# Optimization experiments

Measured on AMD Instinct MI355X. Metric: run time of the kernel, lower is better.

## Reference

```python
import jax, jax.numpy as jnp
import numpy as np

C = 1024
GROUPS = 32
EPS = 1e-5
K = 20


def group_norm(v, weight, bias):
    # v: [B, C]; normalize per group of C//GROUPS channels (torch GroupNorm on 2D input)
    B = v.shape[0]
    g = v.reshape(B, GROUPS, C // GROUPS)
    mean = g.mean(axis=-1, keepdims=True)
    var = g.var(axis=-1, keepdims=True)
    g = (g - mean) * jax.lax.rsqrt(var + EPS)
    return g.reshape(B, C) * weight + bias


def setup_inputs() -> dict:
    key = jax.random.key(0)
    ks = jax.random.split(key, 16)
    B, L = 32, 2048
    s = 1.0 / np.sqrt(C)
    inp = {
        "x": jax.random.normal(ks[0], (B, L, C), dtype=jnp.float32),
        "W": jax.random.uniform(ks[1], (C, C), jnp.float32, -s, s),
        "b": jax.random.uniform(ks[2], (C,), jnp.float32, -s, s),
        "W1": jax.random.uniform(ks[3], (C, C), jnp.float32, -s, s),
        "b1": jax.random.uniform(ks[4], (C,), jnp.float32, -s, s),
        "Wm": jax.random.uniform(ks[5], (C, C), jnp.float32, -s, s),
        "bm": jax.random.uniform(ks[6], (C,), jnp.float32, -s, s),
        "Wa": jax.random.uniform(ks[7], (C, C), jnp.float32, -s, s),
        "ba": jax.random.uniform(ks[8], (C,), jnp.float32, -s, s),
        "g1_w": jnp.ones((C,), jnp.float32),
        "g1_b": jnp.zeros((C,), jnp.float32),
        "g2_w": jnp.ones((C,), jnp.float32),
        "g2_b": jnp.zeros((C,), jnp.float32),
    }
    return inp


def reference(x, W, b, W1, b1, Wm, bm, Wa, ba, g1_w, g1_b, g2_w, g2_b):
    # x: [B, L, C]
    x = jnp.einsum('blc,dc->bld', x, W) + b          # self.linear
    x_M = x.mean(axis=1)                              # adaptive avg pool over L -> [B, C]
    x_M = group_norm(x_M @ Wm.T + bm, g1_w, g1_b)     # linear_max + gn1
    x_A = x.max(axis=1)                               # adaptive max pool over L -> [B, C]
    x_A = group_norm(x_A @ Wa.T + ba, g2_w, g2_b)     # linear_Aug + gn2
    x = jnp.einsum('blc,dc->bld', x, W1) + b1         # self.linear1
    out1 = jnp.einsum('blc,bc->bl', x, x_M)           # x @ x_M^T, squeezed
    out2 = jnp.einsum('blc,bc->bl', x, x_A)
    out = jax.nn.softmax(out1, axis=1) * jax.nn.softmax(out2, axis=1)  # [B, L]
    _, topk_idx = jax.lax.top_k(out, K)               # [B, K]
    selected = jnp.take_along_axis(x, topk_idx[:, :, None], axis=1)  # [B, K, C]
    return selected
```

## Files before the change

### kernel.cpp

```cpp
#include <hip/hip_runtime.h>

#define L_SEQ 2048
#define CH    1024
#define NB    32
#define KSEL  20

typedef short v8s  __attribute__((ext_vector_type(8)));
typedef float v16f __attribute__((ext_vector_type(16)));

#define WS_XSUM   0
#define WS_YMAX   32768
#define WS_M1     65536
#define WS_AMAX   98304
#define WS_T1     131072
#define WS_T2     163840
#define WS_P      196608
#define WS_V      294912
#define WS_S      327680
#define WS_TOPK   393216
#define WS_BC     394240
#define WS_WC     395264
#define WS_WPAK   1443840
#define WS_WTPAK  2492416

__device__ __forceinline__ void split8(float4 qa, float4 qb, uint4& hi, uint4& lo) {
  float f[8] = {qa.x, qa.y, qa.z, qa.w, qb.x, qb.y, qb.z, qb.w};
  unsigned h[8], l[8];
  #pragma unroll
  for (int e = 0; e < 8; ++e) {
    unsigned u  = __float_as_uint(f[e]);
    unsigned hu = u & 0xFFFF0000u;
    float lf    = f[e] - __uint_as_float(hu);
    h[e] = u >> 16;
    l[e] = __float_as_uint(lf) >> 16;
  }
  hi.x = h[0] | (h[1] << 16); hi.y = h[2] | (h[3] << 16);
  hi.z = h[4] | (h[5] << 16); hi.w = h[6] | (h[7] << 16);
  lo.x = l[0] | (l[1] << 16); lo.y = l[2] | (l[3] << 16);
  lo.z = l[4] | (l[5] << 16); lo.w = l[6] | (l[7] << 16);
}

__device__ __forceinline__ void pack_row_body(const float* __restrict__ W,
                                              uint4* __restrict__ wp,
                                              int Rw, int kt, int t) {
  const float* wb = W + (size_t)Rw * 128 * CH;
  uint4* out = wp + ((size_t)Rw * 32 + kt) * 1024;
  #pragma unroll
  for (int pass = 0; pass < 2; ++pass) {
    int idx = pass * 256 + t;
    int r = idx >> 2, p = idx & 3;
    const float* ap = wb + (size_t)r * CH + kt * 32 + p * 8;
    float4 f0 = *(const float4*)ap;
    float4 f1 = *(const float4*)(ap + 4);
    uint4 hi, lo;
    split8(f0, f1, hi, lo);
    int slot = ((r >> 5) * 2 + (p >> 1)) * 128 + (p & 1) * 32 + (r & 31);
    out[slot] = hi;
    out[slot + 64] = lo;
  }
}

__device__ __forceinline__ void pack_tr_body(const float* __restrict__ W,
                                             uint4* __restrict__ wtp,
                                             int cc, int kt, int t,
                                             float (*__restrict__ Wl)[129]) {
  #pragma unroll
  for (int it = 0; it < 16; ++it) {
    int idx = it * 256 + t;
    int el = idx >> 7, cl = idx & 127;
    Wl[el][cl] = W[(size_t)(kt * 32 + el) * CH + cc * 128 + cl];
  }
  __syncthreads();
  uint4* out = wtp + ((size_t)cc * 32 + kt) * 1024;
  #pragma unroll
  for (int pass = 0; pass < 2; ++pass) {
    int sid = pass * 256 + t;
    int r = sid >> 2, p = sid & 3;
    float f[8];
    #pragma unroll
    for (int q = 0; q < 8; ++q) f[q] = Wl[p * 8 + q][r];
    float4 f0 = {f[0], f[1], f[2], f[3]}, f1 = {f[4], f[5], f[6], f[7]};
    uint4 hi, lo;
    split8(f0, f1, hi, lo);
    int slot = ((r >> 5) * 2 + (p >> 1)) * 128 + (p & 1) * 32 + (r & 31);
    out[slot] = hi;
    out[slot + 64] = lo;
  }
}

__global__ __launch_bounds__(256) void prep_kernel(const float* __restrict__ W,
                                                   const float* __restrict__ W1,
                                                   const float* __restrict__ b,
                                                   const float* __restrict__ b1,
                                                   uint4* __restrict__ wp,
                                                   uint4* __restrict__ wtp,
                                                   float* __restrict__ wsf,
                                                   float* __restrict__ bc) {
  __shared__ float Wl[32][129];
  int t = threadIdx.x, x = blockIdx.x, y = blockIdx.y;
  if (y < 8) {
    int flat = (y * 32 + x) * 256 + t;
    wsf[WS_XSUM + flat] = 0.f;
    if (flat < 32768) wsf[WS_V + flat] = 0.f;
    pack_row_body(W, wp, y, x, t);
  } else if (y < 16) {
    int tid = ((y - 8) * 32 + x) * 256 + t;
    float4* wc4 = (float4*)(wsf + WS_WC);
    #pragma unroll
    for (int r = 0; r < 4; ++r) wc4[(size_t)tid * 4 + r] = float4{0.f, 0.f, 0.f, 0.f};
    pack_tr_body(W, wtp, y - 8, x, t, Wl);
  } else {
    int bk = (y - 16) * 32 + x;
    int d = bk * 8 + (t >> 5);
    int lane = t & 31;
    const float4* wr = (const float4*)(W1 + (size_t)d * CH);
    const float4* br = (const float4*)b;
    float acc = 0.f;
    #pragma unroll
    for (int c = lane; c < 256; c += 32) {
      float4 a = wr[c], m = br[c];
      acc += a.x * m.x + a.y * m.y + a.z * m.z + a.w * m.w;
    }
    #pragma unroll
    for (int off = 16; off; off >>= 1) acc += __shfl_xor(acc, off);
    if (lane == 0) bc[d] = acc + b1[d];
  }
}

__global__ __launch_bounds__(256) void packw_kernel(const float* __restrict__ W,
                                                    uint4* __restrict__ wp) {
  pack_row_body(W, wp, blockIdx.y, blockIdx.x, threadIdx.x);
}

__global__ __launch_bounds__(256) void mean_kernel(const float* __restrict__ x,
                                                   float* __restrict__ xsum) {
  int b = blockIdx.y, chunk = blockIdx.x, t = threadIdx.x;
  const float4* bp = (const float4*)(x + ((size_t)b * L_SEQ + (size_t)chunk * 64) * CH);
  float sx = 0.f, sy = 0.f, sz = 0.f, sw = 0.f;
  #pragma unroll 4
  for (int l = 0; l < 64; ++l) {
    float4 a = bp[l * 256 + t];
    sx += a.x; sy += a.y; sz += a.z; sw += a.w;
  }
  float* dst = xsum + b * CH + t * 4;
  atomicAdd(dst + 0, sx); atomicAdd(dst + 1, sy);
  atomicAdd(dst + 2, sz); atomicAdd(dst + 3, sw);
}

template<bool FOURTH, int NKT>
__device__ __forceinline__ void gemm_core(const float* __restrict__ arow,
                                          const uint4* __restrict__ wbB,
                                          const int cgbase,
                                          uint4 (*__restrict__ smA)[1024],
                                          const int w, const int lane,
                                          v16f acc[4][2]) {
  {
    float4 p0 = *(const float4*)(arow);
    float4 p1 = *(const float4*)(arow + 4);
    float4 p2 = *(const float4*)(arow + 16);
    float4 p3 = *(const float4*)(arow + 20);
    uint4 hi, lo;
    split8(p0, p1, hi, lo);
    smA[0][(w * 2 + 0) * 128 + lane] = hi;
    smA[0][(w * 2 + 0) * 128 + 64 + lane] = lo;
    split8(p2, p3, hi, lo);
    smA[0][(w * 2 + 1) * 128 + lane] = hi;
    smA[0][(w * 2 + 1) * 128 + 64 + lane] = lo;
  }
  v8s bc[4], bn[4];
  #pragma unroll
  for (int j = 0; j < 2; ++j) {
    bc[j * 2]     = *(const v8s*)&wbB[((cgbase + j) * 2 + 0) * 128];
    bc[j * 2 + 1] = *(const v8s*)&wbB[((cgbase + j) * 2 + 0) * 128 + 64];
  }
  __syncthreads();

  for (int kt = 0; kt < NKT; ++kt) {
    const int cur = kt & 1;
    float4 q0, q1, q2, q3;
    if (kt < NKT - 1) {
      const float* an = arow + (kt + 1) * 32;
      q0 = *(const float4*)(an);
      q1 = *(const float4*)(an + 4);
      q2 = *(const float4*)(an + 16);
      q3 = *(const float4*)(an + 20);
    }
    #pragma unroll
    for (int s = 0; s < 2; ++s) {
      const int nkt = s ? kt + 1 : kt, ns = s ^ 1;
      if (nkt < NKT) {
        #pragma unroll
        for (int j = 0; j < 2; ++j) {
          bn[j * 2]     = *(const v8s*)&wbB[(size_t)nkt * 1024 + ((cgbase + j) * 2 + ns) * 128];
          bn[j * 2 + 1] = *(const v8s*)&wbB[(size_t)nkt * 1024 + ((cgbase + j) * 2 + ns) * 128 + 64];
        }
      }
      v8s ah[4], al[4];
      #pragma unroll
      for (int i = 0; i < 4; ++i) {
        int base = (i * 2 + s) * 128 + lane;
        ah[i] = *(const v8s*)&smA[cur][base];
        al[i] = *(const v8s*)&smA[cur][base + 64];
      }
      #pragma unroll
      for (int j = 0; j < 2; ++j) {
        v8s bh = bc[j * 2], bl = bc[j * 2 + 1];
        #pragma unroll
        for (int i = 0; i < 4; ++i) {
          acc[i][j] = __builtin_amdgcn_mfma_f32_32x32x16_bf16(ah[i], bh, acc[i][j], 0, 0, 0);
          acc[i][j] = __builtin_amdgcn_mfma_f32_32x32x16_bf16(ah[i], bl, acc[i][j], 0, 0, 0);
          acc[i][j] = __builtin_amdgcn_mfma_f32_32x32x16_bf16(al[i], bh, acc[i][j], 0, 0, 0);
          if (FOURTH)
            acc[i][j] = __builtin_amdgcn_mfma_f32_32x32x16_bf16(al[i], bl, acc[i][j], 0, 0, 0);
        }
      }
      #pragma unroll
      for (int e = 0; e < 4; ++e) bc[e] = bn[e];
    }
    if (kt < NKT - 1) {
      uint4 hi, lo;
      split8(q0, q1, hi, lo);
      smA[cur ^ 1][(w * 2 + 0) * 128 + lane] = hi;
      smA[cur ^ 1][(w * 2 + 0) * 128 + 64 + lane] = lo;
      split8(q2, q3, hi, lo);
      smA[cur ^ 1][(w * 2 + 1) * 128 + lane] = hi;
      smA[cur ^ 1][(w * 2 + 1) * 128 + 64 + lane] = lo;
    }
    __syncthreads();
  }
}

__global__ __launch_bounds__(256, 2) void gemm_max5(const float* __restrict__ X,
                                                    const uint4* __restrict__ wp,
                                                    unsigned* __restrict__ ymax) {
  __shared__ uint4 smA[2][1024];
  const int t = threadIdx.x, lane = t & 63, w = t >> 6;
  const int blk = blockIdx.x;
  const int strip = blk & 3, mt = blk >> 2;
  const int batch = mt >> 4;
  const float* arow = X + (size_t)(mt * 128 + w * 32 + (lane & 31)) * CH + (lane >> 5) * 8;
  v16f acc[4][2];
  #pragma unroll
  for (int i = 0; i < 4; ++i)
    #pragma unroll
    for (int j = 0; j < 2; ++j)
      #pragma unroll
      for (int e = 0; e < 16; ++e) acc[i][j][e] = 0.f;
  const uint4* wbB = wp + (size_t)(strip * 2 + (w >> 1)) * 32768 + lane;
  gemm_core<false, 32>(arow, wbB, (w & 1) * 2, smA, w, lane, acc);

  #pragma unroll
  for (int j = 0; j < 2; ++j) {
    float m = -INFINITY;
    #pragma unroll
    for (int i = 0; i < 4; ++i)
      #pragma unroll
      for (int e = 0; e < 16; ++e) m = fmaxf(m, acc[i][j][e]);
    m = fmaxf(m, __shfl_xor(m, 32));
    if (lane < 32) {
      int col = strip * 256 + w * 64 + j * 32 + lane;
      unsigned u = __float_as_uint(m);
      unsigned enc = (m >= 0.f) ? (u | 0x80000000u) : ~u;
      atomicMax(&ymax[batch * CH + col], enc);
    }
  }
}

__global__ __launch_bounds__(256, 2) void wc_gemm(const float* __restrict__ W1,
                                                  const uint4* __restrict__ wtp,
                                                  float* __restrict__ Wc) {
  __shared__ uint4 smA[2][1024];
  const int t = threadIdx.x, lane = t & 63, w = t >> 6;
  const int blk = blockIdx.x, chunk = blockIdx.y;
  const int strip = blk & 3, mt = blk >> 2;
  const float* arow = W1 + (size_t)(mt * 128 + w * 32 + (lane & 31)) * CH
                         + (lane >> 5) * 8 + chunk * 256;
  v16f acc[4][2];
  #pragma unroll
  for (int i = 0; i < 4; ++i)
    #pragma unroll
    for (int j = 0; j < 2; ++j)
      #pragma unroll
      for (int e = 0; e < 16; ++e) acc[i][j][e] = 0.f;
  const uint4* wbB = wtp + (size_t)(strip * 2 + (w >> 1)) * 32768
                         + (size_t)chunk * (8 * 1024) + lane;
  gemm_core<true, 8>(arow, wbB, (w & 1) * 2, smA, w, lane, acc);

  #pragma unroll
  for (int i = 0; i < 4; ++i)
    #pragma unroll
    for (int j = 0; j < 2; ++j)
      #pragma unroll
      for (int r = 0; r < 16; ++r) {
        int row = (r & 3) + 8 * (r >> 2) + 4 * (lane >> 5);
        int grow = mt * 128 + i * 32 + row;
        int gcol = strip * 256 + w * 64 + j * 32 + (lane & 31);
        atomicAdd(&Wc[(size_t)grow * CH + gcol], acc[i][j][r]);
      }
}

__global__ __launch_bounds__(256, 2) void out_gemm(const float* __restrict__ X,
                                                   const int* __restrict__ idx,
                                                   const uint4* __restrict__ wcp,
                                                   float* __restrict__ C) {
  __shared__ uint4 smA[2][1024];
  const int t = threadIdx.x, lane = t & 63, w = t >> 6;
  const int blk = blockIdx.x, chunk = blockIdx.y;
  const int strip = blk & 3, mt = blk >> 2;
  const int rr = mt * 128 + w * 32 + (lane & 31);
  const int grow_a = (rr / KSEL) * L_SEQ + idx[rr];
  const float* arow = X + (size_t)grow_a * CH + (lane >> 5) * 8 + chunk * 128;
  v16f acc[4][2];
  #pragma unroll
  for (int i = 0; i < 4; ++i)
    #pragma unroll
    for (int j = 0; j < 2; ++j)
      #pragma unroll
      for (int e = 0; e < 16; ++e) acc[i][j][e] = 0.f;
  const uint4* wbB = wcp + (size_t)(strip * 2 + (w >> 1)) * 32768
                         + (size_t)chunk * (4 * 1024) + lane;
  gemm_core<true, 4>(arow, wbB, (w & 1) * 2, smA, w, lane, acc);

  #pragma unroll
  for (int i = 0; i < 4; ++i)
    #pragma unroll
    for (int j = 0; j < 2; ++j)
      #pragma unroll
      for (int r = 0; r < 16; ++r) {
        int row = (r & 3) + 8 * (r >> 2) + 4 * (lane >> 5);
        int grow = mt * 128 + i * 32 + row;
        int gcol = strip * 256 + w * 64 + j * 32 + (lane & 31);
        atomicAdd(&C[(size_t)grow * CH + gcol], acc[i][j][r]);
      }
}

__global__ __launch_bounds__(256) void poolmix_kernel(const float* __restrict__ xsum,
                                                      const unsigned* __restrict__ ymax,
                                                      const float* __restrict__ W,
                                                      const float* __restrict__ bias,
                                                      float* __restrict__ m1,
                                                      float* __restrict__ amax) {
  int t = threadIdx.x;
  int id = blockIdx.x * 256 + t;
  unsigned u = ymax[id];
  float f = (u & 0x80000000u) ? __uint_as_float(u & 0x7FFFFFFFu) : __uint_as_float(~u);
  amax[id] = f + bias[id & (CH - 1)];

  int d = blockIdx.x * 8 + (t >> 5);
  int b = t & 31;
  const float4* Ir = (const float4*)(xsum + b * CH);
  const float4* Mr = (const float4*)(W + (size_t)d * CH);
  float acc = 0.f;
  #pragma unroll 4
  for (int c = 0; c < CH / 4; ++c) {
    float4 a = Ir[c], m = Mr[c];
    acc += a.x * m.x + a.y * m.y + a.z * m.z + a.w * m.w;
  }
  m1[b * CH + d] = acc * (1.f / 2048.f) + bias[d];
}

__global__ __launch_bounds__(256) void lin2_kernel(const float* __restrict__ m1,
                                                   const float* __restrict__ amax,
                                                   const float* __restrict__ Wm,
                                                   const float* __restrict__ bm,
                                                   const float* __restrict__ Wa,
                                                   const float* __restrict__ ba,
                                                   float* __restrict__ t1,
                                                   float* __restrict__ t2) {
  int t = threadIdx.x;
  int which = blockIdx.x >> 7, bk = blockIdx.x & 127;
  const float* I = which ? amax : m1;
  const float* M = which ? Wa : Wm;
  const float* bb = which ? ba : bm;
  float* O = which ? t2 : t1;
  int d = bk * 8 + (t >> 5);
  int b = t & 31;
  const float4* Ir = (const float4*)(I + b * CH);
  const float4* Mr = (const float4*)(M + (size_t)d * CH);
  float acc = 0.f;
  #pragma unroll 4
  for (int c = 0; c < CH / 4; ++c) {
    float4 a = Ir[c], m = Mr[c];
    acc += a.x * m.x + a.y * m.y + a.z * m.z + a.w * m.w;
  }
  O[b * CH + d] = acc + bb[d];
}

__global__ __launch_bounds__(1024) void gnp_kernel(const float* __restrict__ t1,
                                                   const float* __restrict__ t2,
                                                   const float* __restrict__ g1w, const float* __restrict__ g1b,
                                                   const float* __restrict__ g2w, const float* __restrict__ g2b,
                                                   float* __restrict__ p,
                                                   const float* __restrict__ bc,
                                                   float* __restrict__ dout) {
  int b = blockIdx.x, c = threadIdx.x;
  float v1 = t1[b * CH + c], v2 = t2[b * CH + c];
  float s1 = v1, s2 = v2;
  #pragma unroll
  for (int off = 16; off; off >>= 1) { s1 += __shfl_xor(s1, off); s2 += __shfl_xor(s2, off); }
  float d1 = v1 - s1 * (1.f / 32.f), d2 = v2 - s2 * (1.f / 32.f);
  float q1 = d1 * d1, q2 = d2 * d2;
  #pragma unroll
  for (int off = 16; off; off >>= 1) { q1 += __shfl_xor(q1, off); q2 += __shfl_xor(q2, off); }
  float o1 = d1 * rsqrtf(q1 * (1.f / 32.f) + 1e-5f) * g1w[c] + g1b[c];
  float o2 = d2 * rsqrtf(q2 * (1.f / 32.f) + 1e-5f) * g2w[c] + g2b[c];
  p[b * CH + c] = o1 + o2;

  int g = b * CH + c;
  float bcc = bc[c];
  #pragma unroll
  for (int r = 0; r < KSEL; ++r) dout[(size_t)r * (NB * CH) + g] = bcc;
}

__global__ __launch_bounds__(256) void colmm_kernel(const float* __restrict__ S,
                                                    const float* __restrict__ M,
                                                    float* __restrict__ O) {
  __shared__ float Sl[128][32];
  int t = threadIdx.x;
  int e0 = (blockIdx.x & 3) * 256, c0 = (blockIdx.x >> 2) * 128;
  for (int i = t; i < 4096; i += 256) {
    int c = i >> 5, b = i & 31;
    Sl[c][b] = S[b * CH + c0 + c];
  }
  __syncthreads();
  int e = e0 + t;
  float acc[32];
  #pragma unroll
  for (int b = 0; b < 32; ++b) acc[b] = 0.f;
  for (int c = 0; c < 128; ++c) {
    float wv = M[(size_t)(c0 + c) * CH + e];
    #pragma unroll
    for (int b = 0; b < 32; ++b) acc[b] += Sl[c][b] * wv;
  }
  #pragma unroll
  for (int b = 0; b < 32; ++b) atomicAdd(&O[b * CH + e], acc[b]);
}

__global__ __launch_bounds__(256) void logits_kernel(const float* __restrict__ x,
                                                     const float* __restrict__ v,
                                                     float* __restrict__ s) {
  __shared__ float4 vl[256];
  int b = blockIdx.y, chunk = blockIdx.x, t = threadIdx.x;
  vl[t] = ((const float4*)(v + b * CH))[t];
  __syncthreads();
  int wv = t >> 6, lane = t & 63;
  for (int it = 0; it < 8; ++it) {
    int l = chunk * 32 + it * 4 + wv;
    const float4* xr = (const float4*)(x + ((size_t)b * L_SEQ + l) * CH);
    float acc = 0.f;
    #pragma unroll
    for (int rep = 0; rep < 4; ++rep) {
      float4 a = xr[rep * 64 + lane];
      float4 c = vl[rep * 64 + lane];
      acc += a.x * c.x + a.y * c.y + a.z * c.z + a.w * c.w;
    }
    #pragma unroll
    for (int off = 32; off; off >>= 1) acc += __shfl_xor(acc, off);
    if (lane == 0) s[b * L_SEQ + l] = acc;
  }
}

__global__ __launch_bounds__(256) void topk_kernel(const float* __restrict__ s,
                                                   int* __restrict__ idx_out) {
  int b = blockIdx.x, t = threadIdx.x;
  int lane = t & 63, w = t >> 6;
  __shared__ float lv[4];
  __shared__ int   li[4];
  float v[8];
  #pragma unroll
  for (int j = 0; j < 8; ++j) v[j] = s[b * L_SEQ + j * 256 + t];
  for (int k = 0; k < KSEL; ++k) {
    float bv = -INFINITY; int bi = 1 << 30;
    #pragma unroll
    for (int j = 0; j < 8; ++j) {
      int gi = j * 256 + t;
      if (v[j] > bv || (v[j] == bv && gi < bi)) { bv = v[j]; bi = gi; }
    }
    #pragma unroll
    for (int off = 32; off; off >>= 1) {
      float ov = __shfl_xor(bv, off); int oi = __shfl_xor(bi, off);
      if (ov > bv || (ov == bv && oi < bi)) { bv = ov; bi = oi; }
    }
    if (lane == 0) { lv[w] = bv; li[w] = bi; }
    __syncthreads();
    float fv = lv[0]; int fi = li[0];
    #pragma unroll
    for (int w2 = 1; w2 < 4; ++w2) {
      float ov = lv[w2]; int oi = li[w2];
      if (ov > fv || (ov == fv && oi < fi)) { fv = ov; fi = oi; }
    }
    if (t == 0) idx_out[b * KSEL + k] = fi;
    if ((fi & 255) == t) v[fi >> 8] = -INFINITY;
    __syncthreads();
  }
}

extern "C" void kernel_launch(void* const* d_in, const int* in_sizes, int n_in,
                              void* d_out, int out_size, void* d_ws, size_t ws_size,
                              hipStream_t stream) {
  const float* x   = (const float*)d_in[0];
  const float* W   = (const float*)d_in[1];
  const float* b   = (const float*)d_in[2];
  const float* W1  = (const float*)d_in[3];
  const float* b1  = (const float*)d_in[4];
  const float* Wm  = (const float*)d_in[5];
  const float* bm  = (const float*)d_in[6];
  const float* Wa  = (const float*)d_in[7];
  const float* ba  = (const float*)d_in[8];
  const float* g1w = (const float*)d_in[9];
  const float* g1b = (const float*)d_in[10];
  const float* g2w = (const float*)d_in[11];
  const float* g2b = (const float*)d_in[12];

  float* wsf = (float*)d_ws;
  float*    xsum = wsf + WS_XSUM;
  unsigned* ymax = (unsigned*)(wsf + WS_YMAX);
  float*    m1   = wsf + WS_M1;
  float*    amax = wsf + WS_AMAX;
  float*    t1   = wsf + WS_T1;
  float*    t2   = wsf + WS_T2;
  float*    p    = wsf + WS_P;
  float*    vvec = wsf + WS_V;
  float*    sbuf = wsf + WS_S;
  int*      tidx = (int*)(wsf + WS_TOPK);
  float*    bcv  = wsf + WS_BC;
  float*    Wc   = wsf + WS_WC;
  uint4*    wpak = (uint4*)(wsf + WS_WPAK);
  uint4*    wtpak = (uint4*)(wsf + WS_WTPAK);

  prep_kernel<<<dim3(32, 20), 256, 0, stream>>>(W, W1, b, b1, wpak, wtpak, wsf, bcv);
  mean_kernel<<<dim3(32, 32), 256, 0, stream>>>(x, xsum);
  gemm_max5<<<2048, 256, 0, stream>>>(x, wpak, ymax);

  wc_gemm<<<dim3(32, 4), 256, 0, stream>>>(W1, wtpak, Wc);
  packw_kernel<<<dim3(32, 8), 256, 0, stream>>>(Wc, wtpak);

  poolmix_kernel<<<128, 256, 0, stream>>>(xsum, ymax, W, b, m1, amax);
  lin2_kernel<<<256, 256, 0, stream>>>(m1, amax, Wm, bm, Wa, ba, t1, t2);
  gnp_kernel<<<32, 1024, 0, stream>>>(t1, t2, g1w, g1b, g2w, g2b, p, bcv, (float*)d_out);
  colmm_kernel<<<32, 256, 0, stream>>>(p, Wc, vvec);
  logits_kernel<<<dim3(64, 32), 256, 0, stream>>>(x, vvec, sbuf);
  topk_kernel<<<32, 256, 0, stream>>>(sbuf, tidx);
  out_gemm<<<dim3(20, 8), 256, 0, stream>>>(x, tidx, wtpak, (float*)d_out);
}
```

Before: 963.0 us.

## Merge mean, max-GEMM and Wc GEMM into one interleaved launch; fuse pack with poolmix

Three independent kernels (the column-sum of x, the projected max GEMM, and the W1*W product GEMM) become one 3200-block launch. Each group of 25 blocks holds 16 GEMM tiles, 8 mean chunks and 1 Wc tile, so the bandwidth-bound and MFMA-bound work share the GPU at the same time. The Wc packing and the pooled-linear kernel are merged into a second launch. Inside the GEMM core, the next A-tile is now written to shared memory after the first k-substep instead of after the whole inner loop. This gives earlier LDS writes and somewhat more overlap, at the cost of heterogeneous blocks that may unbalance occupancy and register use.

```diff
diff --git a/kernel.cpp b/kernel.cpp
--- a/kernel.cpp
+++ b/kernel.cpp
@@ -125,26 +125,6 @@
     for (int off = 16; off; off >>= 1) acc += __shfl_xor(acc, off);
     if (lane == 0) bc[d] = acc + b1[d];
   }
-}
-
-__global__ __launch_bounds__(256) void packw_kernel(const float* __restrict__ W,
-                                                    uint4* __restrict__ wp) {
-  pack_row_body(W, wp, blockIdx.y, blockIdx.x, threadIdx.x);
-}
-
-__global__ __launch_bounds__(256) void mean_kernel(const float* __restrict__ x,
-                                                   float* __restrict__ xsum) {
-  int b = blockIdx.y, chunk = blockIdx.x, t = threadIdx.x;
-  const float4* bp = (const float4*)(x + ((size_t)b * L_SEQ + (size_t)chunk * 64) * CH);
-  float sx = 0.f, sy = 0.f, sz = 0.f, sw = 0.f;
-  #pragma unroll 4
-  for (int l = 0; l < 64; ++l) {
-    float4 a = bp[l * 256 + t];
-    sx += a.x; sy += a.y; sz += a.z; sw += a.w;
-  }
-  float* dst = xsum + b * CH + t * 4;
-  atomicAdd(dst + 0, sx); atomicAdd(dst + 1, sy);
-  atomicAdd(dst + 2, sz); atomicAdd(dst + 3, sw);
 }
 
 template<bool FOURTH, int NKT>
@@ -216,87 +196,104 @@
       }
       #pragma unroll
       for (int e = 0; e < 4; ++e) bc[e] = bn[e];
-    }
-    if (kt < NKT - 1) {
-      uint4 hi, lo;
-      split8(q0, q1, hi, lo);
-      smA[cur ^ 1][(w * 2 + 0) * 128 + lane] = hi;
-      smA[cur ^ 1][(w * 2 + 0) * 128 + 64 + lane] = lo;
-      split8(q2, q3, hi, lo);
-      smA[cur ^ 1][(w * 2 + 1) * 128 + lane] = hi;
-      smA[cur ^ 1][(w * 2 + 1) * 128 + 64 + lane] = lo;
+      if (s == 0 && kt < NKT - 1) {
+        uint4 hi, lo;
+        split8(q0, q1, hi, lo);
+        smA[cur ^ 1][(w * 2 + 0) * 128 + lane] = hi;
+        smA[cur ^ 1][(w * 2 + 0) * 128 + 64 + lane] = lo;
+        split8(q2, q3, hi, lo);
+        smA[cur ^ 1][(w * 2 + 1) * 128 + lane] = hi;
+        smA[cur ^ 1][(w * 2 + 1) * 128 + 64 + lane] = lo;
+      }
     }
     __syncthreads();
   }
 }
 
-__global__ __launch_bounds__(256, 2) void gemm_max5(const float* __restrict__ X,
-                                                    const uint4* __restrict__ wp,
-                                                    unsigned* __restrict__ ymax) {
+__global__ __launch_bounds__(256, 2) void fused3_kernel(const float* __restrict__ X,
+                                                        const uint4* __restrict__ wp,
+                                                        unsigned* __restrict__ ymax,
+                                                        float* __restrict__ xsum,
+                                                        const float* __restrict__ W1,
+                                                        const uint4* __restrict__ wtp,
+                                                        float* __restrict__ Wc) {
   __shared__ uint4 smA[2][1024];
+  const int id = blockIdx.x;
+  const int g = id / 25, r = id % 25;
   const int t = threadIdx.x, lane = t & 63, w = t >> 6;
-  const int blk = blockIdx.x;
-  const int strip = blk & 3, mt = blk >> 2;
-  const int batch = mt >> 4;
-  const float* arow = X + (size_t)(mt * 128 + w * 32 + (lane & 31)) * CH + (lane >> 5) * 8;
-  v16f acc[4][2];
-  #pragma unroll
-  for (int i = 0; i < 4; ++i)
-    #pragma unroll
-    for (int j = 0; j < 2; ++j)
-      #pragma unroll
-      for (int e = 0; e < 16; ++e) acc[i][j][e] = 0.f;
-  const uint4* wbB = wp + (size_t)(strip * 2 + (w >> 1)) * 32768 + lane;
-  gemm_core<false, 32>(arow, wbB, (w & 1) * 2, smA, w, lane, acc);
-
-  #pragma unroll
-  for (int j = 0; j < 2; ++j) {
-    float m = -INFINITY;
+
+  if (r < 16) {
+    const int k = g * 16 + r;
+    const int strip = k & 3, mt = k >> 2;
+    const int batch = mt >> 4;
+    const float* arow = X + (size_t)(mt * 128 + w * 32 + (lane & 31)) * CH + (lane >> 5) * 8;
+    v16f acc[4][2];
     #pragma unroll
     for (int i = 0; i < 4; ++i)
       #pragma unroll
-      for (int e = 0; e < 16; ++e) m = fmaxf(m, acc[i][j][e]);
-    m = fmaxf(m, __shfl_xor(m, 32));
-    if (lane < 32) {
-      int col = strip * 256 + w * 64 + j * 32 + lane;
-      unsigned u = __float_as_uint(m);
-      unsigned enc = (m >= 0.f) ? (u | 0x80000000u) : ~u;
-      atomicMax(&ymax[batch * CH + col], enc);
-    }
-  }
-}
-
-__global__ __launch_bounds__(256, 2) void wc_gemm(const float* __restrict__ W1,
-                                                  const uint4* __restrict__ wtp,
-                                                  float* __restrict__ Wc) {
-  __shared__ uint4 smA[2][1024];
-  const int t = threadIdx.x, lane = t & 63, w = t >> 6;
-  const int blk = blockIdx.x, chunk = blockIdx.y;
-  const int strip = blk & 3, mt = blk >> 2;
-  const float* arow = W1 + (size_t)(mt * 128 + w * 32 + (lane & 31)) * CH
-                         + (lane >> 5) * 8 + chunk * 256;
-  v16f acc[4][2];
-  #pragma unroll
-  for (int i = 0; i < 4; ++i)
-    #pragma unroll
-    for (int j = 0; j < 2; ++j)
-      #pragma unroll
-      for (int e = 0; e < 16; ++e) acc[i][j][e] = 0.f;
-  const uint4* wbB = wtp + (size_t)(strip * 2 + (w >> 1)) * 32768
-                         + (size_t)chunk * (8 * 1024) + lane;
-  gemm_core<true, 8>(arow, wbB, (w & 1) * 2, smA, w, lane, acc);
-
-  #pragma unroll
-  for (int i = 0; i < 4; ++i)
-    #pragma unroll
-    for (int j = 0; j < 2; ++j)
-      #pragma unroll
-      for (int r = 0; r < 16; ++r) {
-        int row = (r & 3) + 8 * (r >> 2) + 4 * (lane >> 5);
-        int grow = mt * 128 + i * 32 + row;
-        int gcol = strip * 256 + w * 64 + j * 32 + (lane & 31);
-        atomicAdd(&Wc[(size_t)grow * CH + gcol], acc[i][j][r]);
+      for (int j = 0; j < 2; ++j)
+        #pragma unroll
+        for (int e = 0; e < 16; ++e) acc[i][j][e] = 0.f;
+    const uint4* wbB = wp + (size_t)(strip * 2 + (w >> 1)) * 32768 + lane;
+    gemm_core<false, 32>(arow, wbB, (w & 1) * 2, smA, w, lane, acc);
+
+    #pragma unroll
+    for (int j = 0; j < 2; ++j) {
+      float m = -INFINITY;
+      #pragma unroll
+      for (int i = 0; i < 4; ++i)
+        #pragma unroll
+        for (int e = 0; e < 16; ++e) m = fmaxf(m, acc[i][j][e]);
+      m = fmaxf(m, __shfl_xor(m, 32));
+      if (lane < 32) {
+        int col = strip * 256 + w * 64 + j * 32 + lane;
+        unsigned u = __float_as_uint(m);
+        unsigned enc = (m >= 0.f) ? (u | 0x80000000u) : ~u;
+        atomicMax(&ymax[batch * CH + col], enc);
       }
+    }
+  } else if (r < 24) {
+    const int m = g * 8 + (r - 16);
+    const int b = m >> 5, chunk = m & 31;
+    const float4* bp = (const float4*)(X + ((size_t)b * L_SEQ + (size_t)chunk * 64) * CH);
+    float sx = 0.f, sy = 0.f, sz = 0.f, sw = 0.f;
+    #pragma unroll 4
+    for (int l = 0; l < 64; ++l) {
+      float4 a = bp[l * 256 + t];
+      sx += a.x; sy += a.y; sz += a.z; sw += a.w;
+    }
+    float* dst = xsum + b * CH + t * 4;
+    atomicAdd(dst + 0, sx); atomicAdd(dst + 1, sy);
+    atomicAdd(dst + 2, sz); atomicAdd(dst + 3, sw);
+  } else {
+    const int c = g;
+    const int blk = c >> 2, chunk = c & 3;
+    const int strip = blk & 3, mt = blk >> 2;
+    const float* arow = W1 + (size_t)(mt * 128 + w * 32 + (lane & 31)) * CH
+                           + (lane >> 5) * 8 + chunk * 256;
+    v16f acc[4][2];
+    #pragma unroll
+    for (int i = 0; i < 4; ++i)
+      #pragma unroll
+      for (int j = 0; j < 2; ++j)
+        #pragma unroll
+        for (int e = 0; e < 16; ++e) acc[i][j][e] = 0.f;
+    const uint4* wbB = wtp + (size_t)(strip * 2 + (w >> 1)) * 32768
+                           + (size_t)chunk * (8 * 1024) + lane;
+    gemm_core<true, 8>(arow, wbB, (w & 1) * 2, smA, w, lane, acc);
+
+    #pragma unroll
+    for (int i = 0; i < 4; ++i)
+      #pragma unroll
+      for (int j = 0; j < 2; ++j)
+        #pragma unroll
+        for (int rr = 0; rr < 16; ++rr) {
+          int row = (rr & 3) + 8 * (rr >> 2) + 4 * (lane >> 5);
+          int grow = mt * 128 + i * 32 + row;
+          int gcol = strip * 256 + w * 64 + j * 32 + (lane & 31);
+          atomicAdd(&Wc[(size_t)grow * CH + gcol], acc[i][j][rr]);
+        }
+  }
 }
 
 __global__ __launch_bounds__(256, 2) void out_gemm(const float* __restrict__ X,
@@ -334,29 +331,36 @@
       }
 }
 
-__global__ __launch_bounds__(256) void poolmix_kernel(const float* __restrict__ xsum,
-                                                      const unsigned* __restrict__ ymax,
-                                                      const float* __restrict__ W,
-                                                      const float* __restrict__ bias,
-                                                      float* __restrict__ m1,
-                                                      float* __restrict__ amax) {
-  int t = threadIdx.x;
-  int id = blockIdx.x * 256 + t;
-  unsigned u = ymax[id];
-  float f = (u & 0x80000000u) ? __uint_as_float(u & 0x7FFFFFFFu) : __uint_as_float(~u);
-  amax[id] = f + bias[id & (CH - 1)];
-
-  int d = blockIdx.x * 8 + (t >> 5);
-  int b = t & 31;
-  const float4* Ir = (const float4*)(xsum + b * CH);
-  const float4* Mr = (const float4*)(W + (size_t)d * CH);
-  float acc = 0.f;
-  #pragma unroll 4
-  for (int c = 0; c < CH / 4; ++c) {
-    float4 a = Ir[c], m = Mr[c];
-    acc += a.x * m.x + a.y * m.y + a.z * m.z + a.w * m.w;
-  }
-  m1[b * CH + d] = acc * (1.f / 2048.f) + bias[d];
+__global__ __launch_bounds__(256) void mid_kernel(const float* __restrict__ Wc,
+                                                  uint4* __restrict__ wtp,
+                                                  const float* __restrict__ xsum,
+                                                  const unsigned* __restrict__ ymax,
+                                                  const float* __restrict__ W,
+                                                  const float* __restrict__ bias,
+                                                  float* __restrict__ m1,
+                                                  float* __restrict__ amax) {
+  int id = blockIdx.x, t = threadIdx.x;
+  if (id < 256) {
+    pack_row_body(Wc, wtp, id >> 5, id & 31, t);
+  } else {
+    int bk = id - 256;
+    int iid = bk * 256 + t;
+    unsigned u = ymax[iid];
+    float f = (u & 0x80000000u) ? __uint_as_float(u & 0x7FFFFFFFu) : __uint_as_float(~u);
+    amax[iid] = f + bias[iid & (CH - 1)];
+
+    int d = bk * 8 + (t >> 5);
+    int b = t & 31;
+    const float4* Ir = (const float4*)(xsum + b * CH);
+    const float4* Mr = (const float4*)(W + (size_t)d * CH);
+    float acc = 0.f;
+    #pragma unroll 4
+    for (int c = 0; c < CH / 4; ++c) {
+      float4 a = Ir[c], m = Mr[c];
+      acc += a.x * m.x + a.y * m.y + a.z * m.z + a.w * m.w;
+    }
+    m1[b * CH + d] = acc * (1.f / 2048.f) + bias[d];
+  }
 }
 
 __global__ __launch_bounds__(256) void lin2_kernel(const float* __restrict__ m1,
@@ -529,13 +533,9 @@
   uint4*    wtpak = (uint4*)(wsf + WS_WTPAK);
 
   prep_kernel<<<dim3(32, 20), 256, 0, stream>>>(W, W1, b, b1, wpak, wtpak, wsf, bcv);
-  mean_kernel<<<dim3(32, 32), 256, 0, stream>>>(x, xsum);
-  gemm_max5<<<2048, 256, 0, stream>>>(x, wpak, ymax);
-
-  wc_gemm<<<dim3(32, 4), 256, 0, stream>>>(W1, wtpak, Wc);
-  packw_kernel<<<dim3(32, 8), 256, 0, stream>>>(Wc, wtpak);
-
-  poolmix_kernel<<<128, 256, 0, stream>>>(xsum, ymax, W, b, m1, amax);
+  fused3_kernel<<<3200, 256, 0, stream>>>(x, wpak, ymax, xsum, W1, wtpak, Wc);
+  mid_kernel<<<384, 256, 0, stream>>>(Wc, wtpak, xsum, ymax, W, b, m1, amax);
+
   lin2_kernel<<<256, 256, 0, stream>>>(m1, amax, Wm, bm, Wa, ba, t1, t2);
   gnp_kernel<<<32, 1024, 0, stream>>>(t1, t2, g1w, g1b, g2w, g2b, p, bcv, (float*)d_out);
   colmm_kernel<<<32, 256, 0, stream>>>(p, Wc, vvec);
```

After: 919.2 us. -4.5%, faster.
